# Kernel optimization log

Hardware: AMD Instinct MI355X
Metric: run time of the kernel (lower is better)

Reference implementation:

```python
import jax, jax.numpy as jnp
import numpy as np
from jax import lax

K = 9  # propagation kernel

def conv(x, w, b, pad):
    y = lax.conv_general_dilated(x, w, (1, 1), [(pad, pad), (pad, pad)],
                                 dimension_numbers=('NCHW', 'OIHW', 'NCHW'))
    return y + b[None, :, None, None]

def bn(x, g, beta):
    # SynchronizedBatchNorm2d in eval mode with identity running stats (mean=0, var=1)
    return x * g[None, :, None, None] + beta[None, :, None, None]

def propagate(deep, wts):
    # Dynamic local filtering (same math as img2col * weights, sum over 81 taps),
    # computed as 81 shifted-slice FMAs instead of materializing the (n,c,hw,81) tensor.
    p = K // 2
    n, c, h, w = deep.shape
    padded = jnp.pad(deep, ((0, 0), (0, 0), (p, p), (p, p)))
    out = jnp.zeros_like(deep)
    for k in range(K * K):  # k = dy*9 + dx, matching unfold(2).unfold(3) flattening
        dy, dx = k // K, k % K
        out = out + padded[:, :, dy:dy + h, dx:dx + w] * wts[:, k:k + 1]
    return out

def setup_inputs():
    key = jax.random.key(0)
    ks = jax.random.split(key, 40)
    N, C, H, W = 1, 256, 96, 192
    NUM_CLASSES = 19
    s = 0.05
    f32 = jnp.float32
    d = {}
    d['f1_deep'] = jax.random.normal(ks[0], (N, C, H, W), f32)
    d['f1_low'] = jax.random.normal(ks[1], (N, C, H, W), f32)
    d['f2_low'] = jax.random.normal(ks[2], (N, C, H, W), f32)
    # WeightPredictor
    d['wp_c1_w'] = jax.random.normal(ks[3], (256, 256, 3, 3), f32) * s
    d['wp_c1_b'] = jnp.zeros((256,), f32)
    d['wp_c2_w'] = jax.random.normal(ks[4], (256, 512, 3, 3), f32) * s
    d['wp_c2_b'] = jnp.zeros((256,), f32)
    d['wp_fc_w'] = jax.random.normal(ks[5], (81, 256, 1, 1), f32) * s
    d['wp_fc_b'] = jnp.zeros((81,), f32)
    # AdaptiveScheduler
    d['sch_c1_w'] = jax.random.normal(ks[6], (256, 256, 3, 3), f32) * s
    d['sch_c1_b'] = jnp.zeros((256,), f32)
    d['sch_c2_w'] = jax.random.normal(ks[7], (256, 256, 3, 3), f32) * s
    d['sch_c2_b'] = jnp.zeros((256,), f32)
    d['sch_fc_w'] = jax.random.normal(ks[8], (1, 256), f32) * s
    d['sch_fc_b'] = jnp.zeros((1,), f32)
    # AdaptNet
    d['ad_c1_w'] = jax.random.normal(ks[9], (256, 512, 3, 3), f32) * s
    d['ad_c1_b'] = jnp.zeros((256,), f32)
    d['ad_c2_w'] = jax.random.normal(ks[10], (256, 256, 3, 3), f32) * s
    d['ad_c2_b'] = jnp.zeros((256,), f32)
    d['ad_c3_w'] = jax.random.normal(ks[11], (256, 256, 3, 3), f32) * s
    d['ad_c3_b'] = jnp.zeros((256,), f32)
    # reduce_conv2 (1x1 conv + BN)
    d['rc_w'] = jax.random.normal(ks[12], (48, 256, 1, 1), f32) * s
    d['rc_b'] = jnp.zeros((48,), f32)
    d['rc_g'] = jnp.ones((48,), f32)
    d['rc_beta'] = jnp.zeros((48,), f32)
    # last_conv
    d['lc1_w'] = jax.random.normal(ks[13], (256, 304, 3, 3), f32) * s
    d['lc1_b'] = jnp.zeros((256,), f32)
    d['lc1_g'] = jnp.ones((256,), f32)
    d['lc1_beta'] = jnp.zeros((256,), f32)
    d['lc2_w'] = jax.random.normal(ks[14], (256, 256, 3, 3), f32) * s
    d['lc2_b'] = jnp.zeros((256,), f32)
    d['lc2_g'] = jnp.ones((256,), f32)
    d['lc2_beta'] = jnp.zeros((256,), f32)
    d['lc3_w'] = jax.random.normal(ks[15], (NUM_CLASSES, 256, 1, 1), f32) * s
    d['lc3_b'] = jnp.zeros((NUM_CLASSES,), f32)
    return d

def reference(f1_deep, f1_low, f2_low,
              wp_c1_w, wp_c1_b, wp_c2_w, wp_c2_b, wp_fc_w, wp_fc_b,
              sch_c1_w, sch_c1_b, sch_c2_w, sch_c2_b, sch_fc_w, sch_fc_b,
              ad_c1_w, ad_c1_b, ad_c2_w, ad_c2_b, ad_c3_w, ad_c3_b,
              rc_w, rc_b, rc_g, rc_beta,
              lc1_w, lc1_b, lc1_g, lc1_beta,
              lc2_w, lc2_b, lc2_g, lc2_beta,
              lc3_w, lc3_b):
    n, c, h, w = f1_deep.shape
    # WeightPredictor: shared conv1 applied to both low features, cat, conv2, 1x1, softmax over 81 taps
    a1 = conv(f1_low, wp_c1_w, wp_c1_b, 1)
    a2 = conv(f2_low, wp_c1_w, wp_c1_b, 1)
    f = conv(jnp.concatenate([a1, a2], axis=1), wp_c2_w, wp_c2_b, 1)
    kernel = jax.nn.softmax(conv(f, wp_fc_w, wp_fc_b, 0), axis=1)  # (n,81,h,w)
    # AdaptiveScheduler
    diff = conv(f1_low, sch_c1_w, sch_c1_b, 1) - conv(f2_low, sch_c1_w, sch_c1_b, 1)
    o = conv(diff, sch_c2_w, sch_c2_b, 1)
    pooled = jnp.mean(o, axis=(2, 3)).squeeze()  # (256,) since n=1
    deviation = pooled @ sch_fc_w.T + sch_fc_b  # (1,)
    # PropagationModule (dynamic 9x9 local filtering of f1_deep by predicted per-pixel kernel)
    prop = propagate(f1_deep, kernel)  # (n,256,h,w)
    # AdaptNet
    x = conv(jnp.concatenate([f2_low, prop], axis=1), ad_c1_w, ad_c1_b, 1)
    x = conv(x, ad_c2_w, ad_c2_b, 1)
    x = conv(x, ad_c3_w, ad_c3_b, 1)
    # reduce_conv2 + last_conv
    low = bn(conv(f2_low, rc_w, rc_b, 0), rc_g, rc_beta)  # (n,48,h,w)
    x = jnp.concatenate([x, low], axis=1)  # (n,304,h,w)
    x = bn(conv(x, lc1_w, lc1_b, 1), lc1_g, lc1_beta)
    x = bn(conv(x, lc2_w, lc2_b, 1), lc2_g, lc2_beta)
    x = conv(x, lc3_w, lc3_b, 0)  # (n,19,h,w)
    out = jax.image.resize(x, (x.shape[0], x.shape[1], 4 * h, 4 * w), method='bilinear')
    return (out, deviation)
```

## Files before the change

kernel.cpp:

```cpp
#include <hip/hip_runtime.h>
#include <math.h>

#define HWIMG 18432
#define W2 194
#define H2 98
#define NPX1 (H2 * W2)
#define W4 200
#define H4 104
#define NPX4 (H4 * W4)
#define NOUT (19 * 384 * 768)

typedef short bf16x8 __attribute__((ext_vector_type(8)));
typedef float f32x16 __attribute__((ext_vector_type(16)));

__device__ __forceinline__ ushort bf16r(float f) {
    union { float f; unsigned u; } a; a.f = f;
    unsigned u = a.u;
    return (ushort)((u + 0x7fffu + ((u >> 16) & 1u)) >> 16);
}
__device__ __forceinline__ float b2f(ushort u) {
    union { unsigned i; float f; } a; a.i = ((unsigned)u) << 16;
    return a.f;
}
__device__ __forceinline__ bf16x8 ld8(const ushort* p) {
    return *reinterpret_cast<const bf16x8*>(p);
}

__device__ __forceinline__ void gld16(const ushort* g, ushort* l) {
    __builtin_amdgcn_global_load_lds(
        (const __attribute__((address_space(1))) unsigned int*)g,
        (__attribute__((address_space(3))) unsigned int*)l, 16, 0, 0);
}

#define MF(a, b, c) __builtin_amdgcn_mfma_f32_32x32x16_bf16(a, b, c, 0, 0, 0)

__device__ __forceinline__ int swz(int L) { return L ^ (((L >> 7) & 7) << 4); }


__global__ __launch_bounds__(256) void xform_t_k(const float* __restrict__ src,
                                                 const float* __restrict__ src2,
                                                 ushort* __restrict__ dst)
{
    const int px = blockIdx.x * 32 + (threadIdx.x & 31);
    const int c8 = (blockIdx.y * 8 + (threadIdx.x >> 5)) * 8;
    if (px >= NPX1) return;
    const int yP = px / W2, xP = px % W2;
    const int y = yP - 1, x = xP - 1;
    ushort v[8];
    if (y >= 0 && y < 96 && x >= 0 && x < 192) {
        const int p = y * 192 + x;
#pragma unroll
        for (int j = 0; j < 8; ++j) {
            float f = src[(size_t)(c8 + j) * HWIMG + p];
            if (src2) f -= src2[(size_t)(c8 + j) * HWIMG + p];
            v[j] = bf16r(f);
        }
    } else {
#pragma unroll
        for (int j = 0; j < 8; ++j) v[j] = 0;
    }
    *reinterpret_cast<uint4*>(dst + ((size_t)(c8 >> 4) * NPX1 + px) * 16 + (c8 & 15))
        = *reinterpret_cast<uint4*>(v);
}

__global__ __launch_bounds__(256) void xform_nhwc_k(const float* __restrict__ src,
                                                    ushort* __restrict__ dst)
{
    const int px = blockIdx.x * 8 + (threadIdx.x >> 5);
    const int c8 = (threadIdx.x & 31) * 8;
    if (px >= NPX4) return;
    const int yP = px / W4, xP = px % W4;
    const int y = yP - 4, x = xP - 4;
    ushort v[8];
    if (y >= 0 && y < 96 && x >= 0 && x < 192) {
        const int p = y * 192 + x;
#pragma unroll
        for (int j = 0; j < 8; ++j) v[j] = bf16r(src[(size_t)(c8 + j) * HWIMG + p]);
    } else {
#pragma unroll
        for (int j = 0; j < 8; ++j) v[j] = 0;
    }
    *reinterpret_cast<uint4*>(dst + (size_t)px * 256 + c8) = *reinterpret_cast<uint4*>(v);
}

__global__ __launch_bounds__(256) void borderzero3_k(ushort* __restrict__ b0,
                                                     ushort* __restrict__ b1,
                                                     ushort* __restrict__ b2)
{
    ushort* buf = (blockIdx.y == 0) ? b0 : ((blockIdx.y == 1) ? b1 : b2);
    const int idx = blockIdx.x * 256 + threadIdx.x;
    if (idx >= 580 * 16) return;
    const int pi = idx % 580;
    const int cb = idx / 580;
    int pp;
    if (pi < 194) pp = pi;
    else if (pi < 388) pp = 97 * 194 + (pi - 194);
    else if (pi < 484) pp = (pi - 388 + 1) * 194;
    else pp = (pi - 484 + 1) * 194 + 193;
    uint4 z = {0, 0, 0, 0};
    ushort* p = buf + ((size_t)cb * NPX1 + pp) * 16;
    *reinterpret_cast<uint4*>(p) = z;
    *reinterpret_cast<uint4*>(p + 8) = z;
}

struct WtxJob {
    const float* w; const float* b; const float* g; const float* beta;
    int CoutR, Coutp, CinR0, kb0e, CinR1, KBt, ntaps, wtoff, biasoff;
};

__global__ __launch_bounds__(256) void wtx_multi_k(WtxJob J0, WtxJob J1, WtxJob J2,
                                                   WtxJob J3, WtxJob J4, WtxJob J5,
                                                   ushort* __restrict__ wt,
                                                   float* __restrict__ biasout)
{
    WtxJob J = J0;
    switch (blockIdx.y) {
        case 1: J = J1; break; case 2: J = J2; break; case 3: J = J3; break;
        case 4: J = J4; break; case 5: J = J5; break; default: break;
    }
    const int idx = blockIdx.x * 256 + threadIdx.x;
    const int total = J.ntaps * J.KBt * J.Coutp * 16;
    const int CinT = J.CinR0 + J.CinR1;
    if (idx < total) {
        const int c16 = idx & 15;
        const int oc = (idx >> 4) % J.Coutp;
        const int r2 = idx / (16 * J.Coutp);
        const int tap = r2 % J.ntaps;
        const int kbt = r2 / J.ntaps;
        const int k = kbt * 16 + c16;
        float val = 0.f;
        if (oc < J.CoutR) {
            int cit = -1;
            if (k < J.kb0e) { if (k < J.CinR0) cit = k; }
            else { const int k1 = k - J.kb0e; if (k1 < J.CinR1) cit = J.CinR0 + k1; }
            if (cit >= 0) {
                val = J.w[((size_t)oc * CinT + cit) * J.ntaps + tap];
                if (J.g) val *= J.g[oc];
            }
        }
        wt[J.wtoff + idx] = bf16r(val);
    } else if (idx < total + J.Coutp) {
        const int oc = idx - total;
        float v = 0.f;
        if (oc < J.CoutR) {
            v = J.b ? J.b[oc] : 0.f;
            if (J.g) v = v * J.g[oc] + J.beta[oc];
        }
        biasout[J.biasoff + oc] = v;
    }
}

struct ConvJob {
    const ushort* in0; const ushort* in1;
    int KB0, KB1;
    const ushort* wt;
    const float* bias;
    ushort* out;
    int CoutWr;
};

template<int NTAPS>
__device__ __forceinline__ void stage_kb(
    const ConvJob& J, int kb, char* Ab, char* Bb,
    int y0, int x0, int ocb0, int Coutp, int tid, int b_r, int b_h8, int wu)
{
    constexpr int AROWS = (NTAPS == 9) ? 4 : 2;
    constexpr int AW = (NTAPS == 9) ? 66 : 64;
    constexpr int ASLOTS = AROWS * AW * 2;
    const ushort* plane = (kb < J.KB0)
        ? (J.in0 + (size_t)kb * (NPX1 * 16))
        : (J.in1 + (size_t)(kb - J.KB0) * (NPX1 * 16));
#pragma unroll
    for (int i = 0; i < (ASLOTS + 127) / 128; ++i) {
        const int f16 = i * 128 + tid;
        if ((ASLOTS % 128 == 0) || (f16 < ASLOTS)) {
            const int L = swz(f16 * 16);
            const int e = L >> 5;
            const int h8 = ((L >> 4) & 1) * 8;
            const int r = e / AW;
            const int xx = e - r * AW;
            const int px = (NTAPS == 9)
                ? (y0 - 1 + r) * W2 + (x0 - 1 + xx)
                : (y0 + r) * W2 + (x0 + xx);
            const ushort* src = plane + (size_t)px * 16 + h8;
            const int wub = (f16 & ~63) * 16;
            gld16(src, (ushort*)(Ab + __builtin_amdgcn_readfirstlane(wub)));
        }
    }
    const ushort* wsrc = J.wt + ((size_t)kb * NTAPS * Coutp + ocb0 + b_r) * 16 + b_h8;
#pragma unroll
    for (int t = 0; t < NTAPS; ++t) {
        gld16(wsrc + (size_t)t * Coutp * 16, (ushort*)(Bb + t * 2048 + wu));
    }
}

template<int NTAPS>
__global__ __launch_bounds__(128) void conv_lds_k(ConvJob j0, ConvJob j1, ConvJob j2,
                                                  int Coutp)
{
    constexpr int AROWS = (NTAPS == 9) ? 4 : 2;
    constexpr int AW = (NTAPS == 9) ? 66 : 64;
    constexpr int ABYTES = AROWS * AW * 32;
    constexpr int BBYTES = NTAPS * 64 * 32;
    __shared__ __align__(128) char Abuf[2][ABYTES];
    __shared__ __align__(128) char Bbuf[2][BBYTES];

    ConvJob J = j0;
    if (blockIdx.y == 1) J = j1;
    else if (blockIdx.y == 2) J = j2;

    const int nblk = gridDim.x;
    const int cpx = nblk >> 3;
    const int sw = ((int)blockIdx.x & 7) * cpx + ((int)blockIdx.x >> 3);
    const int pt = sw % 144;
    const int ocb0 = (sw / 144) * 64;
    const int y0 = (pt / 3) * 2 + 1;
    const int x0 = (pt % 3) * 64 + 1;

    const int tid = threadIdx.x;
    const int lane = tid & 63;
    const int wm = tid >> 6;
    const int l31 = lane & 31;
    const int h16 = (lane >> 5) * 16;

    const int bl = swz(tid * 16);
    const int b_r = bl >> 5;
    const int b_h8 = ((bl >> 4) & 1) * 8;
    const int wu = __builtin_amdgcn_readfirstlane((tid & ~63) * 16);

    const int KBtot = J.KB0 + J.KB1;

    f32x16 c00 = {}, c01 = {}, c10 = {}, c11 = {};

    stage_kb<NTAPS>(J, 0, Abuf[0], Bbuf[0], y0, x0, ocb0, Coutp, tid, b_r, b_h8, wu);

    int cur = 0;
    for (int kb = 0; kb < KBtot; ++kb) {
        __syncthreads();
        if (kb + 1 < KBtot)
            stage_kb<NTAPS>(J, kb + 1, Abuf[cur ^ 1], Bbuf[cur ^ 1],
                            y0, x0, ocb0, Coutp, tid, b_r, b_h8, wu);
        const char* Ab = Abuf[cur];
        const char* Bb = Bbuf[cur];
#pragma unroll
        for (int t = 0; t < NTAPS; ++t) {
            int entA;
            if (NTAPS == 9) entA = (wm + t / 3) * AW + (t % 3) + l31;
            else            entA = wm * 64 + l31;
            const int SA = swz(entA * 32 + h16);
            bf16x8 a0 = ld8((const ushort*)(Ab + SA));
            bf16x8 a1 = ld8((const ushort*)(Ab + SA + 1024));
            const int SB = swz((t * 64 + l31) * 32 + h16);
            bf16x8 b0 = ld8((const ushort*)(Bb + SB));
            bf16x8 b1 = ld8((const ushort*)(Bb + SB + 1024));
            c00 = MF(a0, b0, c00);
            c01 = MF(a0, b1, c01);
            c10 = MF(a1, b0, c10);
            c11 = MF(a1, b1, c11);
        }
        cur ^= 1;
    }

    const int pxbase = (y0 + wm) * W2 + x0;
    const int rlo = (lane >> 5) * 4;
#pragma unroll
    for (int j = 0; j < 2; ++j) {
        if (ocb0 + j * 32 + 32 > J.CoutWr) continue;
        const int oc = ocb0 + j * 32 + l31;
        const float bs = J.bias[oc];
        const size_t obase = (size_t)(oc >> 4) * ((size_t)NPX1 * 16) + (oc & 15);
        const f32x16 v0 = j ? c01 : c00;
        const f32x16 v1 = j ? c11 : c10;
#pragma unroll
        for (int r = 0; r < 16; ++r) {
            const int rw = (r & 3) + 8 * (r >> 2) + rlo;
            J.out[obase + (size_t)(pxbase + rw) * 16] = bf16r(v0[r] + bs);
            J.out[obase + (size_t)(pxbase + 32 + rw) * 16] = bf16r(v1[r] + bs);
        }
    }
}

__global__ __launch_bounds__(256) void softmax81_k(ushort* __restrict__ t)
{
    const int p = blockIdx.x * 256 + threadIdx.x;
    if (p >= HWIMG) return;
    const int y = p / 192, x = p % 192;
    const size_t pp = (size_t)(y + 1) * W2 + (x + 1);
    float v[81];
    float m = -1e30f;
#pragma unroll
    for (int k = 0; k < 81; ++k) {
        v[k] = b2f(t[((size_t)(k >> 4) * NPX1 + pp) * 16 + (k & 15)]);
        m = fmaxf(m, v[k]);
    }
    float s = 0.f;
#pragma unroll
    for (int k = 0; k < 81; ++k) { v[k] = __expf(v[k] - m); s += v[k]; }
    const float inv = 1.f / s;
#pragma unroll
    for (int k = 0; k < 81; ++k)
        t[((size_t)(k >> 4) * NPX1 + pp) * 16 + (k & 15)] = bf16r(v[k] * inv);
}

__global__ __launch_bounds__(256) void prop_k(const ushort* __restrict__ deep,
                                              const ushort* __restrict__ ker,
                                              ushort* __restrict__ out)
{
    __shared__ float kl[8][81];
    const int pxb = blockIdx.x * 8;
    const int t = threadIdx.x;
    for (int i = t; i < 8 * 81; i += 256) {
        const int pp = pxb + i / 81, k = i % 81;
        float kv = 0.f;
        if (pp < NPX1) {
            const int yP = pp / W2, xP = pp % W2;
            if (yP >= 1 && yP <= 96 && xP >= 1 && xP <= 192)
                kv = b2f(ker[((size_t)(k >> 4) * NPX1 + pp) * 16 + (k & 15)]);
        }
        kl[i / 81][k] = kv;
    }
    __syncthreads();
    const int pi = t >> 5;
    const int c8 = (t & 31) * 8;
    const int pp = pxb + pi;
    if (pp >= NPX1) return;
    const int yP = pp / W2, xP = pp % W2;
    ushort* op = out + ((size_t)(c8 >> 4) * NPX1 + pp) * 16 + (c8 & 15);
    if (yP < 1 || yP > 96 || xP < 1 || xP > 192) {
        uint4 z = {0, 0, 0, 0};
        *reinterpret_cast<uint4*>(op) = z;
        return;
    }
    const int y = yP - 1, x = xP - 1;
    float acc[8];
#pragma unroll
    for (int j = 0; j < 8; ++j) acc[j] = 0.f;
    const ushort* dbase = deep + ((size_t)(y + 4) * W4 + (x + 4)) * 256 + c8;
#pragma unroll
    for (int k = 0; k < 81; ++k) {
        const int dy = k / 9 - 4, dx = k % 9 - 4;
        const float kv = kl[pi][k];
        bf16x8 d = ld8(dbase + (ptrdiff_t)(dy * W4 + dx) * 256);
#pragma unroll
        for (int j = 0; j < 8; ++j) acc[j] += b2f((ushort)d[j]) * kv;
    }
    ushort v[8];
#pragma unroll
    for (int j = 0; j < 8; ++j) v[j] = bf16r(acc[j]);
    *reinterpret_cast<uint4*>(op) = *reinterpret_cast<uint4*>(v);
}

__global__ __launch_bounds__(256) void rowsum_k(const ushort* __restrict__ t,
                                                float* __restrict__ partial)
{
    const int y = blockIdx.x >> 2;
    const int bx = blockIdx.x & 3;
    const int c = threadIdx.x;
    const size_t base = ((size_t)(c >> 4) * NPX1 + (size_t)(y + 1) * W2 + 1 + bx * 48) * 16
                      + (c & 15);
    float s = 0.f;
    for (int x = 0; x < 48; ++x) s += b2f(t[base + (size_t)x * 16]);
    partial[(size_t)blockIdx.x * 256 + c] = s;
}

__global__ __launch_bounds__(256) void dev_k(const float* __restrict__ partial,
                                             const float* __restrict__ fcw,
                                             const float* __restrict__ fcb,
                                             float* __restrict__ o)
{
    __shared__ float buf[256];
    const int c = threadIdx.x;
    float s = 0.f;
    for (int i = 0; i < 384; ++i) s += partial[(size_t)i * 256 + c];
    buf[c] = s * fcw[c];
    __syncthreads();
    for (int st = 128; st > 0; st >>= 1) {
        if (c < st) buf[c] += buf[c + st];
        __syncthreads();
    }
    if (c == 0) o[0] = buf[0] * (1.f / (float)HWIMG) + fcb[0];
}

__global__ __launch_bounds__(256) void upsample_k(const ushort* __restrict__ in,
                                                  float* __restrict__ outp)
{
    const int idx = blockIdx.x * 256 + threadIdx.x;
    if (idx >= NOUT) return;
    const int ox = idx % 768;
    const int t = idx / 768;
    const int oy = t % 384;
    const int c = t / 384;

    const float fx = (ox + 0.5f) * 0.25f - 0.5f;
    const float fy = (oy + 0.5f) * 0.25f - 0.5f;
    const int x0 = (int)floorf(fx);
    const int y0 = (int)floorf(fy);
    const float wx = fx - (float)x0;
    const float wy = fy - (float)y0;
    const int x0c = min(max(x0, 0), 191), x1c = min(max(x0 + 1, 0), 191);
    const int y0c = min(max(y0, 0), 95), y1c = min(max(y0 + 1, 0), 95);

    const size_t cb = (size_t)(c >> 4) * NPX1;
    const int c16 = c & 15;
    const float v00 = b2f(in[(cb + (size_t)(y0c + 1) * W2 + (x0c + 1)) * 16 + c16]);
    const float v01 = b2f(in[(cb + (size_t)(y0c + 1) * W2 + (x1c + 1)) * 16 + c16]);
    const float v10 = b2f(in[(cb + (size_t)(y1c + 1) * W2 + (x0c + 1)) * 16 + c16]);
    const float v11 = b2f(in[(cb + (size_t)(y1c + 1) * W2 + (x1c + 1)) * 16 + c16]);
    outp[idx] = (1.f - wy) * ((1.f - wx) * v00 + wx * v01)
              + wy * ((1.f - wx) * v10 + wx * v11);
}

extern "C" void kernel_launch(void* const* d_in, const int* in_sizes, int n_in,
                              void* d_out, int out_size, void* d_ws, size_t ws_size,
                              hipStream_t stream)
{
    const float* f1_deep = (const float*)d_in[0];
    const float* f1_low  = (const float*)d_in[1];
    const float* f2_low  = (const float*)d_in[2];
    const float* wp_c1_w = (const float*)d_in[3];
    const float* wp_c1_b = (const float*)d_in[4];
    const float* wp_c2_w = (const float*)d_in[5];
    const float* wp_c2_b = (const float*)d_in[6];
    const float* wp_fc_w = (const float*)d_in[7];
    const float* wp_fc_b = (const float*)d_in[8];
    const float* sch_c1_w = (const float*)d_in[9];
    const float* sch_c2_w = (const float*)d_in[11];
    const float* sch_c2_b = (const float*)d_in[12];
    const float* sch_fc_w = (const float*)d_in[13];
    const float* sch_fc_b = (const float*)d_in[14];
    const float* ad_c1_w = (const float*)d_in[15];
    const float* ad_c1_b = (const float*)d_in[16];
    const float* ad_c2_w = (const float*)d_in[17];
    const float* ad_c2_b = (const float*)d_in[18];
    const float* ad_c3_w = (const float*)d_in[19];
    const float* ad_c3_b = (const float*)d_in[20];
    const float* rc_w    = (const float*)d_in[21];
    const float* rc_b    = (const float*)d_in[22];
    const float* rc_g    = (const float*)d_in[23];
    const float* rc_beta = (const float*)d_in[24];
    const float* lc1_w   = (const float*)d_in[25];
    const float* lc1_b   = (const float*)d_in[26];
    const float* lc1_g   = (const float*)d_in[27];
    const float* lc1_beta= (const float*)d_in[28];
    const float* lc2_w   = (const float*)d_in[29];
    const float* lc2_b   = (const float*)d_in[30];
    const float* lc2_g   = (const float*)d_in[31];
    const float* lc2_beta= (const float*)d_in[32];
    const float* lc3_w   = (const float*)d_in[33];
    const float* lc3_b   = (const float*)d_in[34];

    float* out = (float*)d_out;
    ushort* ws0 = (ushort*)d_ws;

    const size_t CBBe  = (size_t)NPX1 * 256;
    const size_t BUF0e = (size_t)NPX4 * 256;

    ushort* Bb = ws0 + BUF0e;
    ushort* Cb = Bb + CBBe;
    ushort* Db = Cb + CBBe;
    ushort* Eb = Db + CBBe;
    ushort* Fb = Eb + CBBe;
    ushort* WT = Fb + CBBe;
    float* BIAS = (float*)(WT + 3719168);
    float* PART = (float*)ws0;
    ushort* L48 = Eb + 6 * (size_t)NPX1 * 16;

    const dim3 b256(256), b128(128);

    xform_t_k<<<dim3(595, 4), b256, 0, stream>>>(f1_low, nullptr, Bb);
    xform_t_k<<<dim3(595, 4), b256, 0, stream>>>(f2_low, nullptr, Cb);
    xform_t_k<<<dim3(595, 4), b256, 0, stream>>>(f1_low, f2_low, Db);
    borderzero3_k<<<dim3(37, 3), b256, 0, stream>>>(ws0, Eb, Fb);

    {
        WtxJob w0 = {wp_c1_w, wp_c1_b, nullptr, nullptr, 256, 256, 256, 256, 0, 16, 9, 0, 0};
        WtxJob w1 = {sch_c1_w, nullptr, nullptr, nullptr, 256, 256, 256, 256, 0, 16, 9, 589824, 256};
        WtxJob w2 = {wp_c2_w, wp_c2_b, nullptr, nullptr, 256, 256, 256, 256, 256, 32, 9, 1179648, 512};
        WtxJob w3 = {sch_c2_w, sch_c2_b, nullptr, nullptr, 256, 256, 256, 256, 0, 16, 9, 2359296, 768};
        WtxJob w4 = {wp_fc_w, wp_fc_b, nullptr, nullptr, 81, 128, 256, 256, 0, 16, 1, 2949120, 1024};
        WtxJob w5 = {rc_w, rc_b, rc_g, rc_beta, 48, 128, 256, 256, 0, 16, 1, 2981888, 1280};
        wtx_multi_k<<<dim3(4610, 6), b256, 0, stream>>>(w0, w1, w2, w3, w4, w5, WT, BIAS);
    }

    {
        ConvJob a0 = {Bb, Bb, 16, 0, WT, BIAS, Eb, 256};
        ConvJob a1 = {Cb, Cb, 16, 0, WT, BIAS, Fb, 256};
        ConvJob a2 = {Db, Db, 16, 0, WT + 589824, BIAS + 256, ws0, 256};
        conv_lds_k<9><<<dim3(576, 3), b128, 0, stream>>>(a0, a1, a2, 256);
    }
    {
        ConvJob a0 = {Eb, Fb, 16, 16, WT + 1179648, BIAS + 512, Db, 256};
        ConvJob a1 = {ws0, ws0, 16, 0, WT + 2359296, BIAS + 768, Bb, 256};
        conv_lds_k<9><<<dim3(576, 2), b128, 0, stream>>>(a0, a1, a0, 256);
    }
    rowsum_k<<<384, b256, 0, stream>>>(Bb, PART);
    dev_k<<<1, b256, 0, stream>>>(PART, sch_fc_w, sch_fc_b, out + NOUT);

    {
        ConvJob a0 = {Db, Db, 16, 0, WT + 2949120, BIAS + 1024, Eb, 96};
        ConvJob a1 = {Cb, Cb, 16, 0, WT + 2981888, BIAS + 1280, L48, 64};
        conv_lds_k<1><<<dim3(288, 2), b128, 0, stream>>>(a0, a1, a0, 128);
    }

    {
        WtxJob w0 = {ad_c1_w, ad_c1_b, nullptr, nullptr, 256, 256, 256, 256, 256, 32, 9, 0, 1536};
        WtxJob w1 = {ad_c2_w, ad_c2_b, nullptr, nullptr, 256, 256, 256, 256, 0, 16, 9, 1179648, 1792};
        WtxJob w2 = {ad_c3_w, ad_c3_b, nullptr, nullptr, 256, 256, 256, 256, 0, 16, 9, 1769472, 2048};
        WtxJob w3 = {lc1_w, lc1_b, lc1_g, lc1_beta, 256, 256, 256, 256, 48, 20, 9, 2359296, 2304};
        WtxJob w4 = {lc2_w, lc2_b, lc2_g, lc2_beta, 256, 256, 256, 256, 0, 16, 9, 3096576, 2560};
        WtxJob w5 = {lc3_w, lc3_b, nullptr, nullptr, 19, 128, 256, 256, 0, 16, 1, 3686400, 2816};
        wtx_multi_k<<<dim3(4610, 6), b256, 0, stream>>>(w0, w1, w2, w3, w4, w5, WT, BIAS);
    }

    softmax81_k<<<72, b256, 0, stream>>>(Eb);
    xform_nhwc_k<<<2600, b256, 0, stream>>>(f1_deep, ws0);
    prop_k<<<2377, b256, 0, stream>>>(ws0, Eb, Fb);

    {
        ConvJob a = {Cb, Fb, 16, 16, WT, BIAS + 1536, Bb, 256};
        conv_lds_k<9><<<dim3(576, 1), b128, 0, stream>>>(a, a, a, 256);
    }
    {
        ConvJob a = {Bb, Bb, 16, 0, WT + 1179648, BIAS + 1792, Db, 256};
        conv_lds_k<9><<<dim3(576, 1), b128, 0, stream>>>(a, a, a, 256);
    }
    {
        ConvJob a = {Db, Db, 16, 0, WT + 1769472, BIAS + 2048, Fb, 256};
        conv_lds_k<9><<<dim3(576, 1), b128, 0, stream>>>(a, a, a, 256);
    }
    {
        ConvJob a = {Fb, L48, 16, 4, WT + 2359296, BIAS + 2304, Bb, 256};
        conv_lds_k<9><<<dim3(576, 1), b128, 0, stream>>>(a, a, a, 256);
    }
    {
        ConvJob a = {Bb, Bb, 16, 0, WT + 3096576, BIAS + 2560, Db, 256};
        conv_lds_k<9><<<dim3(576, 1), b128, 0, stream>>>(a, a, a, 256);
    }
    {
        ConvJob a = {Db, Db, 16, 0, WT + 3686400, BIAS + 2816, Cb, 32};
        conv_lds_k<1><<<dim3(288, 1), b128, 0, stream>>>(a, a, a, 128);
    }

    upsample_k<<<(NOUT + 255) / 256, b256, 0, stream>>>(Cb, out);
}
```

Baseline: 515.4 us.

## Switch conv to 16x16x32 MFMA over paired K-blocks, drop double buffering

The implicit-GEMM conv kernel moves from 32x32x16 MFMA tiles to 16x16x32 tiles. Each iteration now stages two 16-channel K-blocks at once, so one MFMA consumes 32 channels, and each wave keeps a 4x4 grid of 16x16 accumulators. The earlier double-buffered prefetch, which overlapped loading the next block with compute, is replaced by load, sync, compute, sync. This gives deeper K per instruction and fewer, larger loads per barrier, at the cost of no load/compute overlap within a block. The loop also assumes the total K-block count is even.

Result: faster. 498.4 us (-3.3%).

```diff
diff --git a/kernel.cpp b/kernel.cpp
--- a/kernel.cpp
+++ b/kernel.cpp
@@ -11,7 +11,7 @@
 #define NOUT (19 * 384 * 768)
 
 typedef short bf16x8 __attribute__((ext_vector_type(8)));
-typedef float f32x16 __attribute__((ext_vector_type(16)));
+typedef float f32x4 __attribute__((ext_vector_type(4)));
 
 __device__ __forceinline__ ushort bf16r(float f) {
     union { float f; unsigned u; } a; a.f = f;
@@ -32,7 +32,7 @@
         (__attribute__((address_space(3))) unsigned int*)l, 16, 0, 0);
 }
 
-#define MF(a, b, c) __builtin_amdgcn_mfma_f32_32x32x16_bf16(a, b, c, 0, 0, 0)
+#define MF16(a, b, c) __builtin_amdgcn_mfma_f32_16x16x32_bf16(a, b, c, 0, 0, 0)
 
 __device__ __forceinline__ int swz(int L) { return L ^ (((L >> 7) & 7) << 4); }
 
@@ -161,7 +161,7 @@
 
 template<int NTAPS>
 __device__ __forceinline__ void stage_kb(
-    const ConvJob& J, int kb, char* Ab, char* Bb,
+    const ConvJob& J, int kb, int kbh, char* Ab, char* Bb,
     int y0, int x0, int ocb0, int Coutp, int tid, int b_r, int b_h8, int wu)
 {
     constexpr int AROWS = (NTAPS == 9) ? 4 : 2;
@@ -182,15 +182,14 @@
             const int px = (NTAPS == 9)
                 ? (y0 - 1 + r) * W2 + (x0 - 1 + xx)
                 : (y0 + r) * W2 + (x0 + xx);
-            const ushort* src = plane + (size_t)px * 16 + h8;
-            const int wub = (f16 & ~63) * 16;
-            gld16(src, (ushort*)(Ab + __builtin_amdgcn_readfirstlane(wub)));
+            gld16(plane + (size_t)px * 16 + h8,
+                  (ushort*)(Ab + __builtin_amdgcn_readfirstlane((f16 & ~63) * 16)));
         }
     }
     const ushort* wsrc = J.wt + ((size_t)kb * NTAPS * Coutp + ocb0 + b_r) * 16 + b_h8;
 #pragma unroll
     for (int t = 0; t < NTAPS; ++t) {
-        gld16(wsrc + (size_t)t * Coutp * 16, (ushort*)(Bb + t * 2048 + wu));
+        gld16(wsrc + (size_t)t * Coutp * 16, (ushort*)(Bb + (t * 2 + kbh) * 2048 + wu));
     }
 }
 
@@ -200,10 +199,9 @@
 {
     constexpr int AROWS = (NTAPS == 9) ? 4 : 2;
     constexpr int AW = (NTAPS == 9) ? 66 : 64;
-    constexpr int ABYTES = AROWS * AW * 32;
-    constexpr int BBYTES = NTAPS * 64 * 32;
-    __shared__ __align__(128) char Abuf[2][ABYTES];
-    __shared__ __align__(128) char Bbuf[2][BBYTES];
+    constexpr int APLANE = AROWS * AW * 32;
+    __shared__ __align__(1024) char Abuf[2 * APLANE];
+    __shared__ __align__(1024) char Bbuf[NTAPS * 2 * 2048];
 
     ConvJob J = j0;
     if (blockIdx.y == 1) J = j1;
@@ -220,8 +218,9 @@
     const int tid = threadIdx.x;
     const int lane = tid & 63;
     const int wm = tid >> 6;
-    const int l31 = lane & 31;
-    const int h16 = (lane >> 5) * 16;
+    const int l15 = lane & 15;
+    const int kh16 = ((lane >> 4) & 1) * 16;
+    const int pl = lane >> 5;
 
     const int bl = swz(tid * 16);
     const int b_r = bl >> 5;
@@ -230,52 +229,49 @@
 
     const int KBtot = J.KB0 + J.KB1;
 
-    f32x16 c00 = {}, c01 = {}, c10 = {}, c11 = {};
-
-    stage_kb<NTAPS>(J, 0, Abuf[0], Bbuf[0], y0, x0, ocb0, Coutp, tid, b_r, b_h8, wu);
-
-    int cur = 0;
-    for (int kb = 0; kb < KBtot; ++kb) {
+    f32x4 acc[4][4] = {};
+
+    for (int s = 0; s < KBtot; s += 2) {
+        stage_kb<NTAPS>(J, s,     0, Abuf,          Bbuf, y0, x0, ocb0, Coutp, tid, b_r, b_h8, wu);
+        stage_kb<NTAPS>(J, s + 1, 1, Abuf + APLANE, Bbuf, y0, x0, ocb0, Coutp, tid, b_r, b_h8, wu);
         __syncthreads();
-        if (kb + 1 < KBtot)
-            stage_kb<NTAPS>(J, kb + 1, Abuf[cur ^ 1], Bbuf[cur ^ 1],
-                            y0, x0, ocb0, Coutp, tid, b_r, b_h8, wu);
-        const char* Ab = Abuf[cur];
-        const char* Bb = Bbuf[cur];
+
+        const char* Ap = Abuf + pl * APLANE;
 #pragma unroll
         for (int t = 0; t < NTAPS; ++t) {
-            int entA;
-            if (NTAPS == 9) entA = (wm + t / 3) * AW + (t % 3) + l31;
-            else            entA = wm * 64 + l31;
-            const int SA = swz(entA * 32 + h16);
-            bf16x8 a0 = ld8((const ushort*)(Ab + SA));
-            bf16x8 a1 = ld8((const ushort*)(Ab + SA + 1024));
-            const int SB = swz((t * 64 + l31) * 32 + h16);
-            bf16x8 b0 = ld8((const ushort*)(Bb + SB));
-            bf16x8 b1 = ld8((const ushort*)(Bb + SB + 1024));
-            c00 = MF(a0, b0, c00);
-            c01 = MF(a0, b1, c01);
-            c10 = MF(a1, b0, c10);
-            c11 = MF(a1, b1, c11);
-        }
-        cur ^= 1;
+            const int rowb = (NTAPS == 9) ? ((wm + t / 3) * AW + (t % 3)) : (wm * AW);
+            const char* Bp = Bbuf + (t * 2 + pl) * 2048;
+            bf16x8 a[4], b[4];
+#pragma unroll
+            for (int q = 0; q < 4; ++q) {
+                const int la = (rowb + q * 16 + l15) * 32 + kh16;
+                a[q] = ld8((const ushort*)(Ap + swz(la)));
+                const int lb = (q * 16 + l15) * 32 + kh16;
+                b[q] = ld8((const ushort*)(Bp + swz(lb)));
+            }
+#pragma unroll
+            for (int i = 0; i < 4; ++i)
+#pragma unroll
+                for (int j = 0; j < 4; ++j)
+                    acc[i][j] = MF16(a[i], b[j], acc[i][j]);
+        }
+        __syncthreads();
     }
 
     const int pxbase = (y0 + wm) * W2 + x0;
-    const int rlo = (lane >> 5) * 4;
-#pragma unroll
-    for (int j = 0; j < 2; ++j) {
-        if (ocb0 + j * 32 + 32 > J.CoutWr) continue;
-        const int oc = ocb0 + j * 32 + l31;
+    const int r4 = (lane >> 4) * 4;
+#pragma unroll
+    for (int qo = 0; qo < 4; ++qo) {
+        if (ocb0 + qo * 16 + 16 > J.CoutWr) continue;
+        const int oc = ocb0 + qo * 16 + l15;
         const float bs = J.bias[oc];
         const size_t obase = (size_t)(oc >> 4) * ((size_t)NPX1 * 16) + (oc & 15);
-        const f32x16 v0 = j ? c01 : c00;
-        const f32x16 v1 = j ? c11 : c10;
-#pragma unroll
-        for (int r = 0; r < 16; ++r) {
-            const int rw = (r & 3) + 8 * (r >> 2) + rlo;
-            J.out[obase + (size_t)(pxbase + rw) * 16] = bf16r(v0[r] + bs);
-            J.out[obase + (size_t)(pxbase + 32 + rw) * 16] = bf16r(v1[r] + bs);
+#pragma unroll
+        for (int qp = 0; qp < 4; ++qp) {
+            const int pp = pxbase + qp * 16 + r4;
+#pragma unroll
+            for (int r = 0; r < 4; ++r)
+                J.out[obase + (size_t)(pp + r) * 16] = bf16r(acc[qp][qo][r] + bs);
         }
     }
 }
```
